# Performance work log

Hardware: AMD Instinct MI355X
Metric: run time of the kernel (lower is better)

Reference implementation:

```python
import jax, jax.numpy as jnp
import numpy as np

N_NODES = 100000
N_EDGES = 1600000
N_GRAPHS = 64
IN_DIM = 128
PROJ_DIM = 128
HID_DIM = 128


def _gcn_conv(x, src, dst, ew, W, b, n):
    """PyG GCNConv: add self-loops, symmetric normalization, x@W then scatter-sum."""
    loop = jnp.arange(n)
    s = jnp.concatenate([src, loop])
    d = jnp.concatenate([dst, loop])
    w = jnp.concatenate([ew, jnp.ones((n,), dtype=x.dtype)])
    deg = jax.ops.segment_sum(w, d, num_segments=n)  # in-degree incl. self-loops
    dinv = jnp.where(deg > 0, deg ** -0.5, 0.0).astype(x.dtype)
    norm = dinv[s] * w * dinv[d]                      # [E+N]
    h = x @ W                                         # [N, out]
    out = jax.ops.segment_sum(h[s] * norm[:, None], d, num_segments=n)
    return out + b


def setup_inputs() -> dict:
    key = jax.random.key(0)
    ks = jax.random.split(key, 10)
    x = jax.random.normal(ks[0], (N_NODES, IN_DIM), dtype=jnp.float32)
    edge_index = jax.random.randint(ks[1], (2, N_EDGES), 0, N_NODES, dtype=jnp.int64)
    edge_weight = jax.random.uniform(ks[2], (N_EDGES,), dtype=jnp.float32)
    batch = jnp.sort(jax.random.randint(ks[3], (N_NODES,), 0, N_GRAPHS, dtype=jnp.int64))
    # learned parameters (Glorot-ish scaling)
    W1 = jax.random.normal(ks[4], (IN_DIM, PROJ_DIM), dtype=jnp.float32) / np.sqrt(IN_DIM)
    b1 = jnp.zeros((PROJ_DIM,), dtype=jnp.float32)
    W2 = jax.random.normal(ks[5], (PROJ_DIM, HID_DIM), dtype=jnp.float32) / np.sqrt(PROJ_DIM)
    b2 = jnp.zeros((HID_DIM,), dtype=jnp.float32)
    Wfc = jax.random.normal(ks[6], (HID_DIM, HID_DIM), dtype=jnp.float32) / np.sqrt(HID_DIM)
    bfc = jnp.zeros((HID_DIM,), dtype=jnp.float32)
    return {"x": x, "edge_index": edge_index, "edge_weight": edge_weight, "batch": batch,
            "W1": W1, "b1": b1, "W2": W2, "b2": b2, "Wfc": Wfc, "bfc": bfc}


def reference(x, edge_index, edge_weight, batch, W1, b1, W2, b2, Wfc, bfc):
    src, dst = edge_index[0], edge_index[1]
    n = x.shape[0]
    z = _gcn_conv(x, src, dst, edge_weight, W1, b1, n)
    z = jax.nn.relu(z)
    z = _gcn_conv(z, src, dst, edge_weight, W2, b2, n)
    # global mean pool over graph ids
    sums = jax.ops.segment_sum(z, batch, num_segments=N_GRAPHS)          # [G, H]
    cnts = jax.ops.segment_sum(jnp.ones((n,), z.dtype), batch, num_segments=N_GRAPHS)
    pooled = sums / jnp.maximum(cnts, 1.0)[:, None]
    return pooled @ Wfc + bfc
```

## Files before the change

### kernel.cpp

```cpp
#include <hip/hip_runtime.h>
#include <hip/hip_fp16.h>
#include <hip/hip_fp8.h>


constexpr int FDIM = 128;

typedef __attribute__((ext_vector_type(8))) short short8v;
typedef __attribute__((ext_vector_type(4))) float f32x4;
typedef __attribute__((ext_vector_type(2))) float f32x2;

__device__ __forceinline__ ushort f2bf(float f) {
    uint u = __float_as_uint(f);
    return (ushort)((u + 0x7fffu + ((u >> 16) & 1u)) >> 16);
}

#if __has_builtin(__builtin_amdgcn_cvt_pk_f32_fp8) && __has_builtin(__builtin_amdgcn_cvt_pk_fp8_f32)
#define FP8_HW 1
#else
#define FP8_HW 0
#endif

__device__ __forceinline__ void fp8x8_dec(uint2 v, float* f) {
#if FP8_HW
    f32x2 a = __builtin_amdgcn_cvt_pk_f32_fp8(v.x, false);
    f32x2 b = __builtin_amdgcn_cvt_pk_f32_fp8(v.x, true);
    f32x2 c = __builtin_amdgcn_cvt_pk_f32_fp8(v.y, false);
    f32x2 d = __builtin_amdgcn_cvt_pk_f32_fp8(v.y, true);
    f[0] = a[0]; f[1] = a[1]; f[2] = b[0]; f[3] = b[1];
    f[4] = c[0]; f[5] = c[1]; f[6] = d[0]; f[7] = d[1];
#else
    __half2_raw h;
    h = __hip_cvt_fp8x2_to_halfraw2((__hip_fp8x2_storage_t)(v.x & 0xffffu), __HIP_E4M3);
    float2 a = __half22float2(*(__half2*)&h);
    f[0] = a.x; f[1] = a.y;
    h = __hip_cvt_fp8x2_to_halfraw2((__hip_fp8x2_storage_t)(v.x >> 16), __HIP_E4M3);
    a = __half22float2(*(__half2*)&h);
    f[2] = a.x; f[3] = a.y;
    h = __hip_cvt_fp8x2_to_halfraw2((__hip_fp8x2_storage_t)(v.y & 0xffffu), __HIP_E4M3);
    a = __half22float2(*(__half2*)&h);
    f[4] = a.x; f[5] = a.y;
    h = __hip_cvt_fp8x2_to_halfraw2((__hip_fp8x2_storage_t)(v.y >> 16), __HIP_E4M3);
    a = __half22float2(*(__half2*)&h);
    f[6] = a.x; f[7] = a.y;
#endif
}
__device__ __forceinline__ uint2 fp8x8_enc(const float* f) {
#if FP8_HW
    int lo = 0, hi = 0;
    lo = __builtin_amdgcn_cvt_pk_fp8_f32(f[0], f[1], lo, false);
    lo = __builtin_amdgcn_cvt_pk_fp8_f32(f[2], f[3], lo, true);
    hi = __builtin_amdgcn_cvt_pk_fp8_f32(f[4], f[5], hi, false);
    hi = __builtin_amdgcn_cvt_pk_fp8_f32(f[6], f[7], hi, true);
    return make_uint2((uint)lo, (uint)hi);
#else
    uint p0 = __hip_cvt_float2_to_fp8x2(make_float2(f[0], f[1]), __HIP_SATFINITE, __HIP_E4M3);
    uint p1 = __hip_cvt_float2_to_fp8x2(make_float2(f[2], f[3]), __HIP_SATFINITE, __HIP_E4M3);
    uint p2 = __hip_cvt_float2_to_fp8x2(make_float2(f[4], f[5]), __HIP_SATFINITE, __HIP_E4M3);
    uint p3 = __hip_cvt_float2_to_fp8x2(make_float2(f[6], f[7]), __HIP_SATFINITE, __HIP_E4M3);
    return make_uint2(p0 | (p1 << 16), p2 | (p3 << 16));
#endif
}
__device__ __forceinline__ uchar fp8_enc1(float f) {
#if FP8_HW
    return (uchar)((uint)__builtin_amdgcn_cvt_pk_fp8_f32(f, f, 0, false) & 0xffu);
#else
    return (uchar)__hip_cvt_float_to_fp8(f, __HIP_SATFINITE, __HIP_E4M3);
#endif
}

__global__ __launch_bounds__(256) void k_init(unsigned long long* packed,
                                              float* psum, int NN, int PS) {
    int i = blockIdx.x * 256 + threadIdx.x;
    if (i < NN) packed[i] = 0ULL;
    if (i < PS) psum[i] = 0.0f;
}

__global__ __launch_bounds__(256) void k_hist(const int* __restrict__ dst,
                                              const float* __restrict__ ew,
                                              unsigned long long* __restrict__ packed,
                                              ushort* __restrict__ aux, int E) {
    int e = blockIdx.x * 256 + threadIdx.x;
    if (e < E) {
        int d = dst[e];
        uint fix = __float2uint_rn(ew[e] * 16777216.0f);
        unsigned long long old =
            atomicAdd(&packed[d], (1ULL << 32) | (unsigned long long)fix);
        aux[e] = (ushort)(old >> 32);
    }
}

__global__ __launch_bounds__(256) void k_merge(const unsigned long long* __restrict__ packed,
                                               int* __restrict__ cnt,
                                               float* __restrict__ dinv, int NN) {
    int n = blockIdx.x * 256 + threadIdx.x;
    if (n >= NN) return;
    unsigned long long v = packed[n];
    cnt[n] = (int)(v >> 32);
    float deg = 1.0f + (float)(v & 0xffffffffULL) * 5.9604644775390625e-8f;
    dinv[n] = rsqrtf(deg);
}

__global__ __launch_bounds__(256) void k_bsum(const int* __restrict__ cnt, int* bsum, int NN) {
    __shared__ int lds[256];
    int b = blockIdx.x, t = threadIdx.x;
    int base = b * 1024;
    int s = 0;
#pragma unroll
    for (int j = 0; j < 4; j++) {
        int i = base + j * 256 + t;
        if (i < NN) s += cnt[i];
    }
    lds[t] = s;
    __syncthreads();
    for (int off = 128; off > 0; off >>= 1) {
        if (t < off) lds[t] += lds[t + off];
        __syncthreads();
    }
    if (t == 0) bsum[b] = lds[0];
}

__global__ __launch_bounds__(256) void k_btops(const int* bsum, int* boff, int* rowptr,
                                               int NB, int NN) {
    __shared__ int lds[256];
    int t = threadIdx.x;
    if (t < NB) lds[t] = bsum[t];
    __syncthreads();
    if (t == 0) {
        int run = 0;
        for (int i = 0; i < NB; i++) { int v = lds[i]; boff[i] = run; run += v; }
        rowptr[NN] = run;
    }
}

__global__ __launch_bounds__(256) void k_scan(const int* __restrict__ cnt,
                                              const int* __restrict__ boff,
                                              int* rowptr, int NN) {
    __shared__ int lds[2][256];
    int b = blockIdx.x, t = threadIdx.x;
    int base = b * 1024 + t * 4;
    int v[4]; int s = 0;
#pragma unroll
    for (int j = 0; j < 4; j++) { v[j] = (base + j < NN) ? cnt[base + j] : 0; s += v[j]; }
    lds[0][t] = s;
    __syncthreads();
    int cur = 0;
    for (int off = 1; off < 256; off <<= 1) {
        int val = lds[cur][t];
        if (t >= off) val += lds[cur][t - off];
        lds[cur ^ 1][t] = val;
        __syncthreads();
        cur ^= 1;
    }
    int excl = lds[cur][t] - s + boff[b];
#pragma unroll
    for (int j = 0; j < 4; j++) {
        if (base + j < NN) rowptr[base + j] = excl;
        excl += v[j];
    }
}

__global__ __launch_bounds__(256) void k_fill(const int* __restrict__ src,
                                              const int* __restrict__ dst,
                                              const float* __restrict__ ew,
                                              const ushort* __restrict__ aux,
                                              const float* __restrict__ dinv,
                                              const int* __restrict__ rowptr,
                                              uint2* __restrict__ csr, int E) {
    int e = blockIdx.x * 256 + threadIdx.x;
    if (e < E) {
        int d = dst[e], s = src[e];
        float nrm = dinv[s] * ew[e] * dinv[d];
        csr[rowptr[d] + (int)aux[e]] = make_uint2((uint)s, __float_as_uint(nrm));
    }
}

__global__ __launch_bounds__(64) void k_gcnt(const int* __restrict__ batch,
                                             int* __restrict__ gcnt, int NN, int G) {
    int g = threadIdx.x;
    if (g >= G) return;
    auto lb = [&](int v) {
        int lo = 0, hi = NN;
        while (lo < hi) { int mid = (lo + hi) >> 1; if (batch[mid] < v) lo = mid + 1; else hi = mid; }
        return lo;
    };
    gcnt[g] = lb(g + 1) - lb(g);
}

__global__ __launch_bounds__(256) void k_wt(const float* __restrict__ W,
                                            ushort* __restrict__ Wt) {
    int t = threadIdx.x;
    for (int i = t; i < FDIM * FDIM; i += 256) {
        int k = i >> 7, n = i & 127;
        Wt[n * FDIM + k] = f2bf(W[i]);
    }
}

__global__ __launch_bounds__(256) void k_gemm(const float* __restrict__ X,
                                              const ushort* __restrict__ Wt,
                                              uchar* __restrict__ H, int N) {
    int t = threadIdx.x;
    int wave = t >> 6, l = t & 63;
    int m = l & 15, kg = (l >> 4) * 8;
    int r0 = blockIdx.x * 64 + wave * 16;
    int row = r0 + m;
    short8v a[4];
    if (row < N) {
#pragma unroll
        for (int ks = 0; ks < 4; ks++) {
            const float* xp = X + (size_t)row * FDIM + ks * 32 + kg;
            float4 f0 = *(const float4*)xp;
            float4 f1 = *(const float4*)(xp + 4);
            short8v av;
            av[0] = (short)f2bf(f0.x); av[1] = (short)f2bf(f0.y);
            av[2] = (short)f2bf(f0.z); av[3] = (short)f2bf(f0.w);
            av[4] = (short)f2bf(f1.x); av[5] = (short)f2bf(f1.y);
            av[6] = (short)f2bf(f1.z); av[7] = (short)f2bf(f1.w);
            a[ks] = av;
        }
    } else {
#pragma unroll
        for (int ks = 0; ks < 4; ks++) a[ks] = (short8v)0;
    }
    int orow = r0 + (l >> 4) * 4;
#pragma unroll
    for (int c = 0; c < 8; c++) {
        f32x4 acc = {0.f, 0.f, 0.f, 0.f};
#pragma unroll
        for (int ks = 0; ks < 4; ks++) {
            short8v b = *(const short8v*)(Wt + (size_t)(c * 16 + m) * FDIM + ks * 32 + kg);
            acc = __builtin_amdgcn_mfma_f32_16x16x32_bf16(a[ks], b, acc, 0, 0, 0);
        }
#pragma unroll
        for (int j = 0; j < 4; j++)
            if (orow + j < N)
                H[(size_t)(orow + j) * FDIM + c * 16 + m] = fp8_enc1(acc[j]);
    }
}

template <int RELU, int POOL>
__global__ __launch_bounds__(256) void k_agg(const uchar* __restrict__ H,
                                             const int* __restrict__ rowptr,
                                             const uint2* __restrict__ csr,
                                             const float* __restrict__ dinv,
                                             const float* __restrict__ bias,
                                             uchar* __restrict__ Z,
                                             const int* __restrict__ batch,
                                             float* __restrict__ psum, int NN) {
    __shared__ float pool[FDIM];
    int t = threadIdx.x;
    int wave = t >> 6, l = t & 63;
    int eg = l >> 4, li = l & 15;
    int f0 = li * 8;
    int gmin = 0;
    if (POOL) {
        if (t < FDIM) pool[t] = 0.0f;
        gmin = batch[blockIdx.x * 16];
        __syncthreads();
    }

    for (int it = 0; it < 4; ++it) {
        int n = blockIdx.x * 16 + wave * 4 + it;
        if (n >= NN) continue;
        float acc[8];
        if (eg == 0) {
            float di = dinv[n];
            float sw = di * di;
            uint2 hv = *(const uint2*)(H + (size_t)n * FDIM + f0);
            float hf[8];
            fp8x8_dec(hv, hf);
#pragma unroll
            for (int j = 0; j < 8; j++) acc[j] = sw * hf[j];
        } else {
#pragma unroll
            for (int j = 0; j < 8; j++) acc[j] = 0.0f;
        }
        int rs = rowptr[n], re = rowptr[n + 1];
#pragma unroll 2
        for (int e = rs; e < re; e += 8) {
            int i0 = e + eg, i1 = e + 4 + eg;
            int c0 = min(i0, re - 1), c1 = min(i1, re - 1);
            uint2 p0 = csr[c0], p1 = csr[c1];
            int s0 = (int)p0.x, s1 = (int)p1.x;
            float w0 = (i0 < re) ? __uint_as_float(p0.y) : 0.0f;
            float w1 = (i1 < re) ? __uint_as_float(p1.y) : 0.0f;
            uint2 v0 = *(const uint2*)(H + (size_t)s0 * FDIM + f0);
            uint2 v1 = *(const uint2*)(H + (size_t)s1 * FDIM + f0);
            float g0[8], g1[8];
            fp8x8_dec(v0, g0);
            fp8x8_dec(v1, g1);
#pragma unroll
            for (int j = 0; j < 8; j++) {
                acc[j] = fmaf(w0, g0[j], acc[j]);
                acc[j] = fmaf(w1, g1[j], acc[j]);
            }
        }
#pragma unroll
        for (int j = 0; j < 8; j++) {
            acc[j] += __shfl_xor(acc[j], 16);
            acc[j] += __shfl_xor(acc[j], 32);
        }
        if (eg == 0) {
            if (POOL) {
                int g = batch[n];
                if (g == gmin) {
#pragma unroll
                    for (int j = 0; j < 8; j++) atomicAdd(&pool[f0 + j], acc[j]);
                } else {
#pragma unroll
                    for (int j = 0; j < 8; j++) atomicAdd(&psum[g * FDIM + f0 + j], acc[j]);
                }
            } else {
#pragma unroll
                for (int j = 0; j < 8; j++) acc[j] = acc[j] + bias[f0 + j];
                if (RELU) {
#pragma unroll
                    for (int j = 0; j < 8; j++) acc[j] = fmaxf(acc[j], 0.0f);
                }
                *(uint2*)(Z + (size_t)n * FDIM + f0) = fp8x8_enc(acc);
            }
        }
    }
    if (POOL) {
        __syncthreads();
        if (t < FDIM) atomicAdd(&psum[gmin * FDIM + t], pool[t]);
    }
}

__global__ __launch_bounds__(128) void k_fc2(const float* __restrict__ psum,
                                             const int* __restrict__ gcnt,
                                             const float* __restrict__ W2,
                                             const float* __restrict__ b2,
                                             const float* __restrict__ Wfc,
                                             const float* __restrict__ bfc,
                                             float* __restrict__ out) {
    __shared__ float p[FDIM], t1[FDIM];
    int g = blockIdx.x, f = threadIdx.x;
    float c = (float)max(gcnt[g], 1);
    p[f] = psum[g * FDIM + f] / c;
    __syncthreads();
    float acc = b2[f];
#pragma unroll 8
    for (int k = 0; k < FDIM; k++) acc = fmaf(p[k], W2[k * FDIM + f], acc);
    t1[f] = acc;
    __syncthreads();
    float acc2 = bfc[f];
#pragma unroll 8
    for (int k = 0; k < FDIM; k++) acc2 = fmaf(t1[k], Wfc[k * FDIM + f], acc2);
    out[g * FDIM + f] = acc2;
}

extern "C" void kernel_launch(void* const* d_in, const int* in_sizes, int n_in,
                              void* d_out, int out_size, void* d_ws, size_t ws_size,
                              hipStream_t stream) {
    const float* x    = (const float*)d_in[0];
    const int*   ei   = (const int*)d_in[1];
    const float* ew   = (const float*)d_in[2];
    const int*   batch= (const int*)d_in[3];
    const float* W1   = (const float*)d_in[4];
    const float* b1   = (const float*)d_in[5];
    const float* W2   = (const float*)d_in[6];
    const float* b2   = (const float*)d_in[7];
    const float* Wfc  = (const float*)d_in[8];
    const float* bfc  = (const float*)d_in[9];
    float* out = (float*)d_out;

    int E  = in_sizes[2];
    int NN = in_sizes[3];
    int G  = out_size / FDIM;

    const int* src = ei;
    const int* dst = ei + E;

    char* ws = (char*)d_ws;
    size_t off = 0;
    auto alloc = [&](size_t bytes) -> void* {
        void* p = ws + off;
        off = (off + bytes + 255) & ~(size_t)255;
        return p;
    };
    unsigned long long* packed = (unsigned long long*)alloc((size_t)NN * 8);
    ushort* aux    = (ushort*)alloc((size_t)E * 2);
    int*   cnt     = (int*)alloc((size_t)NN * 4);
    float* dinv    = (float*)alloc((size_t)NN * 4);
    int*   rowptr  = (int*)alloc((size_t)(NN + 1) * 4);
    int*   bsumA   = (int*)alloc(256 * 4);
    int*   boffA   = (int*)alloc(256 * 4);
    uint2* csr     = (uint2*)alloc((size_t)E * 8);
    float* psum    = (float*)alloc((size_t)G * FDIM * 4);
    int*   gcnt    = (int*)alloc((size_t)G * 4);
    uchar* Bh      = (uchar*)alloc((size_t)NN * FDIM);
    uchar* Bz      = (uchar*)alloc((size_t)NN * FDIM);
    ushort* Wt1    = (ushort*)alloc((size_t)FDIM * FDIM * 2);
    (void)ws_size; (void)n_in;

    int nbN = (NN + 255) / 256;
    int nbE = (E + 255) / 256;
    int NB  = (NN + 1023) / 1024;

    k_init<<<nbN, 256, 0, stream>>>(packed, psum, NN, G * FDIM);
    k_hist<<<nbE, 256, 0, stream>>>(dst, ew, packed, aux, E);
    k_merge<<<nbN, 256, 0, stream>>>(packed, cnt, dinv, NN);
    k_bsum<<<NB, 256, 0, stream>>>(cnt, bsumA, NN);
    k_btops<<<1, 256, 0, stream>>>(bsumA, boffA, rowptr, NB, NN);
    k_scan<<<NB, 256, 0, stream>>>(cnt, boffA, rowptr, NN);
    k_fill<<<nbE, 256, 0, stream>>>(src, dst, ew, aux, dinv, rowptr, csr, E);
    k_gcnt<<<1, 64, 0, stream>>>(batch, gcnt, NN, G);
    k_wt<<<1, 256, 0, stream>>>(W1, Wt1);

    int nbG = (NN + 63) / 64;
    int nbA = (NN + 15) / 16;
    k_gemm<<<nbG, 256, 0, stream>>>(x, Wt1, Bh, NN);
    k_agg<1, 0><<<nbA, 256, 0, stream>>>(Bh, rowptr, csr, dinv, b1, Bz,
                                         batch, psum, NN);
    k_agg<0, 1><<<nbA, 256, 0, stream>>>(Bz, rowptr, csr, dinv, nullptr, nullptr,
                                         batch, psum, NN);
    k_fc2<<<G, 128, 0, stream>>>(psum, gcnt, W2, b2, Wfc, bfc, out);
}
```

Baseline: 335.9 us.

## Widen aggregation to 16-byte fp8 gathers with software-pipelined edge prefetch

Each lane in the aggregation kernel now handles 16 features per edge with a 128-bit load instead of 8 features with a 64-bit load, so 8 edge groups are processed in parallel per wave instead of 4. The edge loop is restructured into a software pipeline: CSR entries are prefetched three steps ahead and the next feature row one step ahead, overlapping gather latency with decode and FMA. The reduction gains an extra shuffle stage, and per-lane register use doubles for accumulators, which may lower occupancy. With about 16 edges per node, each edge group runs only about two iterations, so the pipeline prologue and clamped redundant loads add relative overhead.

```diff
diff --git a/kernel.cpp b/kernel.cpp
--- a/kernel.cpp
+++ b/kernel.cpp
@@ -20,7 +20,7 @@
 #define FP8_HW 0
 #endif
 
-__device__ __forceinline__ void fp8x8_dec(uint2 v, float* f) {
+__device__ __forceinline__ void fp8x16_dec(uint4 v, float* f) {
 #if FP8_HW
     f32x2 a = __builtin_amdgcn_cvt_pk_f32_fp8(v.x, false);
     f32x2 b = __builtin_amdgcn_cvt_pk_f32_fp8(v.x, true);
@@ -28,36 +28,45 @@
     f32x2 d = __builtin_amdgcn_cvt_pk_f32_fp8(v.y, true);
     f[0] = a[0]; f[1] = a[1]; f[2] = b[0]; f[3] = b[1];
     f[4] = c[0]; f[5] = c[1]; f[6] = d[0]; f[7] = d[1];
+    a = __builtin_amdgcn_cvt_pk_f32_fp8(v.z, false);
+    b = __builtin_amdgcn_cvt_pk_f32_fp8(v.z, true);
+    c = __builtin_amdgcn_cvt_pk_f32_fp8(v.w, false);
+    d = __builtin_amdgcn_cvt_pk_f32_fp8(v.w, true);
+    f[8] = a[0]; f[9] = a[1]; f[10] = b[0]; f[11] = b[1];
+    f[12] = c[0]; f[13] = c[1]; f[14] = d[0]; f[15] = d[1];
 #else
-    __half2_raw h;
-    h = __hip_cvt_fp8x2_to_halfraw2((__hip_fp8x2_storage_t)(v.x & 0xffffu), __HIP_E4M3);
-    float2 a = __half22float2(*(__half2*)&h);
-    f[0] = a.x; f[1] = a.y;
-    h = __hip_cvt_fp8x2_to_halfraw2((__hip_fp8x2_storage_t)(v.x >> 16), __HIP_E4M3);
-    a = __half22float2(*(__half2*)&h);
-    f[2] = a.x; f[3] = a.y;
-    h = __hip_cvt_fp8x2_to_halfraw2((__hip_fp8x2_storage_t)(v.y & 0xffffu), __HIP_E4M3);
-    a = __half22float2(*(__half2*)&h);
-    f[4] = a.x; f[5] = a.y;
-    h = __hip_cvt_fp8x2_to_halfraw2((__hip_fp8x2_storage_t)(v.y >> 16), __HIP_E4M3);
-    a = __half22float2(*(__half2*)&h);
-    f[6] = a.x; f[7] = a.y;
+    for (int k = 0; k < 4; k++) {
+        uint w = (&v.x)[k];
+        __half2_raw h;
+        h = __hip_cvt_fp8x2_to_halfraw2((__hip_fp8x2_storage_t)(w & 0xffffu), __HIP_E4M3);
+        float2 a = __half22float2(*(__half2*)&h);
+        f[k * 4 + 0] = a.x; f[k * 4 + 1] = a.y;
+        h = __hip_cvt_fp8x2_to_halfraw2((__hip_fp8x2_storage_t)(w >> 16), __HIP_E4M3);
+        a = __half22float2(*(__half2*)&h);
+        f[k * 4 + 2] = a.x; f[k * 4 + 3] = a.y;
+    }
 #endif
 }
-__device__ __forceinline__ uint2 fp8x8_enc(const float* f) {
+__device__ __forceinline__ uint4 fp8x16_enc(const float* f) {
 #if FP8_HW
-    int lo = 0, hi = 0;
-    lo = __builtin_amdgcn_cvt_pk_fp8_f32(f[0], f[1], lo, false);
-    lo = __builtin_amdgcn_cvt_pk_fp8_f32(f[2], f[3], lo, true);
-    hi = __builtin_amdgcn_cvt_pk_fp8_f32(f[4], f[5], hi, false);
-    hi = __builtin_amdgcn_cvt_pk_fp8_f32(f[6], f[7], hi, true);
-    return make_uint2((uint)lo, (uint)hi);
+    int w0 = 0, w1 = 0, w2 = 0, w3 = 0;
+    w0 = __builtin_amdgcn_cvt_pk_fp8_f32(f[0], f[1], w0, false);
+    w0 = __builtin_amdgcn_cvt_pk_fp8_f32(f[2], f[3], w0, true);
+    w1 = __builtin_amdgcn_cvt_pk_fp8_f32(f[4], f[5], w1, false);
+    w1 = __builtin_amdgcn_cvt_pk_fp8_f32(f[6], f[7], w1, true);
+    w2 = __builtin_amdgcn_cvt_pk_fp8_f32(f[8], f[9], w2, false);
+    w2 = __builtin_amdgcn_cvt_pk_fp8_f32(f[10], f[11], w2, true);
+    w3 = __builtin_amdgcn_cvt_pk_fp8_f32(f[12], f[13], w3, false);
+    w3 = __builtin_amdgcn_cvt_pk_fp8_f32(f[14], f[15], w3, true);
+    return make_uint4((uint)w0, (uint)w1, (uint)w2, (uint)w3);
 #else
-    uint p0 = __hip_cvt_float2_to_fp8x2(make_float2(f[0], f[1]), __HIP_SATFINITE, __HIP_E4M3);
-    uint p1 = __hip_cvt_float2_to_fp8x2(make_float2(f[2], f[3]), __HIP_SATFINITE, __HIP_E4M3);
-    uint p2 = __hip_cvt_float2_to_fp8x2(make_float2(f[4], f[5]), __HIP_SATFINITE, __HIP_E4M3);
-    uint p3 = __hip_cvt_float2_to_fp8x2(make_float2(f[6], f[7]), __HIP_SATFINITE, __HIP_E4M3);
-    return make_uint2(p0 | (p1 << 16), p2 | (p3 << 16));
+    uint w[4];
+    for (int k = 0; k < 4; k++) {
+        uint p0 = __hip_cvt_float2_to_fp8x2(make_float2(f[k*4+0], f[k*4+1]), __HIP_SATFINITE, __HIP_E4M3);
+        uint p1 = __hip_cvt_float2_to_fp8x2(make_float2(f[k*4+2], f[k*4+3]), __HIP_SATFINITE, __HIP_E4M3);
+        w[k] = p0 | (p1 << 16);
+    }
+    return make_uint4(w[0], w[1], w[2], w[3]);
 #endif
 }
 __device__ __forceinline__ uchar fp8_enc1(float f) {
@@ -249,8 +258,8 @@
     __shared__ float pool[FDIM];
     int t = threadIdx.x;
     int wave = t >> 6, l = t & 63;
-    int eg = l >> 4, li = l & 15;
-    int f0 = li * 8;
+    int sg = l >> 3, li = l & 7;
+    int f0 = li * 16;
     int gmin = 0;
     if (POOL) {
         if (t < FDIM) pool[t] = 0.0f;
@@ -261,62 +270,66 @@
     for (int it = 0; it < 4; ++it) {
         int n = blockIdx.x * 16 + wave * 4 + it;
         if (n >= NN) continue;
-        float acc[8];
-        if (eg == 0) {
+        int rs = rowptr[n], re = rowptr[n + 1];
+        float acc[16];
+        if (sg == 0) {
+            uint4 hv = *(const uint4*)(H + (size_t)n * FDIM + f0);
             float di = dinv[n];
             float sw = di * di;
-            uint2 hv = *(const uint2*)(H + (size_t)n * FDIM + f0);
-            float hf[8];
-            fp8x8_dec(hv, hf);
-#pragma unroll
-            for (int j = 0; j < 8; j++) acc[j] = sw * hf[j];
+            float hf[16];
+            fp8x16_dec(hv, hf);
+#pragma unroll
+            for (int j = 0; j < 16; j++) acc[j] = sw * hf[j];
         } else {
 #pragma unroll
-            for (int j = 0; j < 8; j++) acc[j] = 0.0f;
-        }
-        int rs = rowptr[n], re = rowptr[n + 1];
-#pragma unroll 2
-        for (int e = rs; e < re; e += 8) {
-            int i0 = e + eg, i1 = e + 4 + eg;
-            int c0 = min(i0, re - 1), c1 = min(i1, re - 1);
-            uint2 p0 = csr[c0], p1 = csr[c1];
-            int s0 = (int)p0.x, s1 = (int)p1.x;
-            float w0 = (i0 < re) ? __uint_as_float(p0.y) : 0.0f;
-            float w1 = (i1 < re) ? __uint_as_float(p1.y) : 0.0f;
-            uint2 v0 = *(const uint2*)(H + (size_t)s0 * FDIM + f0);
-            uint2 v1 = *(const uint2*)(H + (size_t)s1 * FDIM + f0);
-            float g0[8], g1[8];
-            fp8x8_dec(v0, g0);
-            fp8x8_dec(v1, g1);
-#pragma unroll
-            for (int j = 0; j < 8; j++) {
-                acc[j] = fmaf(w0, g0[j], acc[j]);
-                acc[j] = fmaf(w1, g1[j], acc[j]);
+            for (int j = 0; j < 16; j++) acc[j] = 0.0f;
+        }
+        if (rs < re) {
+            int last = re - 1;
+            uint2 pd0 = csr[min(rs + sg, last)];
+            uint2 pd1 = csr[min(rs + 8 + sg, last)];
+            uint2 pd2 = csr[min(rs + 16 + sg, last)];
+            uint4 hv0 = *(const uint4*)(H + (size_t)pd0.x * FDIM + f0);
+            float w0 = (rs + sg < re) ? __uint_as_float(pd0.y) : 0.0f;
+            for (int e = rs; e < re; e += 8) {
+                uint2 pd3 = csr[min(e + 24 + sg, last)];
+                uint4 hv1 = hv0;
+                float w1 = 0.0f;
+                if (e + 8 < re) {
+                    hv1 = *(const uint4*)(H + (size_t)pd1.x * FDIM + f0);
+                    w1 = (e + 8 + sg < re) ? __uint_as_float(pd1.y) : 0.0f;
+                }
+                float g[16];
+                fp8x16_dec(hv0, g);
+#pragma unroll
+                for (int j = 0; j < 16; j++) acc[j] = fmaf(w0, g[j], acc[j]);
+                pd0 = pd1; pd1 = pd2; pd2 = pd3; hv0 = hv1; w0 = w1;
             }
         }
 #pragma unroll
-        for (int j = 0; j < 8; j++) {
+        for (int j = 0; j < 16; j++) {
+            acc[j] += __shfl_xor(acc[j], 8);
             acc[j] += __shfl_xor(acc[j], 16);
             acc[j] += __shfl_xor(acc[j], 32);
         }
-        if (eg == 0) {
+        if (sg == 0) {
             if (POOL) {
                 int g = batch[n];
                 if (g == gmin) {
 #pragma unroll
-                    for (int j = 0; j < 8; j++) atomicAdd(&pool[f0 + j], acc[j]);
+                    for (int j = 0; j < 16; j++) atomicAdd(&pool[f0 + j], acc[j]);
                 } else {
 #pragma unroll
-                    for (int j = 0; j < 8; j++) atomicAdd(&psum[g * FDIM + f0 + j], acc[j]);
+                    for (int j = 0; j < 16; j++) atomicAdd(&psum[g * FDIM + f0 + j], acc[j]);
                 }
             } else {
 #pragma unroll
-                for (int j = 0; j < 8; j++) acc[j] = acc[j] + bias[f0 + j];
+                for (int j = 0; j < 16; j++) acc[j] = acc[j] + bias[f0 + j];
                 if (RELU) {
 #pragma unroll
-                    for (int j = 0; j < 8; j++) acc[j] = fmaxf(acc[j], 0.0f);
+                    for (int j = 0; j < 16; j++) acc[j] = fmaxf(acc[j], 0.0f);
                 }
-                *(uint2*)(Z + (size_t)n * FDIM + f0) = fp8x8_enc(acc);
+                *(uint4*)(Z + (size_t)n * FDIM + f0) = fp8x16_enc(acc);
             }
         }
     }
```

After: 377.4 us. 12.3% more time.
